# Kernel optimization log

Hardware: AMD Instinct MI355X
Metric: run time of the kernel (lower is better)

## Reference

```python
import jax, jax.numpy as jnp
import numpy as np

H, W = 160, 480
C_IMG = 256
VFC = [64, 128, 256]
N_PTS = 120000


def setup_inputs() -> dict:
    key = jax.random.key(0)
    ks = jax.random.split(key, 16)
    inp = {}
    inp["img_feat"] = jax.random.normal(ks[0], (C_IMG, H, W), jnp.float32)
    inp["seg_prob"] = jax.random.uniform(ks[1], (1, 2, H, W), jnp.float32)
    for i, c in enumerate(VFC):
        inp[f"voxel_feat{i}"] = jax.random.normal(ks[2 + i], (N_PTS, c), jnp.float32)
        x = jax.random.randint(ks[5 + i], (N_PTS,), 0, W + 1)  # col coord in [0, W]
        y = jax.random.randint(ks[8 + i], (N_PTS,), 0, H + 1)  # row coord in [0, H]
        inp[f"img_grid{i}"] = jnp.stack([x, y], axis=1).astype(jnp.int32)
    inp["red_w0"] = jax.random.normal(ks[11], (VFC[2], VFC[0]), jnp.float32) * 0.05
    inp["red_b0"] = jnp.zeros((VFC[2],), jnp.float32)
    inp["red_w1"] = jax.random.normal(ks[12], (VFC[2], VFC[1]), jnp.float32) * 0.05
    inp["red_b1"] = jnp.zeros((VFC[2],), jnp.float32)
    inp["sb_w"] = jax.random.normal(ks[13], (1, C_IMG + VFC[2], 3, 3), jnp.float32) * 0.02
    inp["sb_b"] = jnp.zeros((1,), jnp.float32)
    return inp


def pts2img(coor, pts_feat):
    # coor: [N,2] int (x, y); torch does coor[:, [1,0]] then grid[y, x] = feat
    c = pts_feat.shape[1]
    grid = jnp.zeros((H + 1, W + 1, c), pts_feat.dtype)
    grid = grid.at[coor[:, 1], coor[:, 0]].set(pts_feat, mode="drop")
    return grid[:-1, :-1].transpose(2, 0, 1)  # [C, H, W]


def reference(img_feat, seg_prob, voxel_feat0, voxel_feat1, voxel_feat2,
              img_grid0, img_grid1, img_grid2,
              red_w0, red_b0, red_w1, red_b1, sb_w, sb_b):
    # seg-gated image features
    enhanced = img_feat * seg_prob[0, 1][None]  # [C_IMG, H, W]

    # level 0: scatter + 1x1 conv (64 -> 256)
    p0 = pts2img(img_grid0, voxel_feat0)
    p0 = jnp.einsum('chw,oc->ohw', p0, red_w0) + red_b0[:, None, None]
    # level 1: scatter + 1x1 conv (128 -> 256)
    p1 = pts2img(img_grid1, voxel_feat1)
    p1 = jnp.einsum('chw,oc->ohw', p1, red_w1) + red_b1[:, None, None]
    # level 2: scatter only (already 256)
    p2 = pts2img(img_grid2, voxel_feat2)
    pt_img = p0 + p1 + p2  # [256, H, W]

    fused = jnp.concatenate([enhanced, pt_img], axis=0)[None]  # [1, 512, H, W]
    conv = jax.lax.conv_general_dilated(
        fused, sb_w, window_strides=(1, 1), padding='SAME',
        dimension_numbers=('NCHW', 'OIHW', 'NCHW'))
    conv = conv + sb_b[None, :, None, None]
    attention_map = jax.nn.sigmoid(conv[0])  # [1, H, W]
    return enhanced * attention_map
```

## Files before the change

kernel.cpp:

```cpp
#include <hip/hip_runtime.h>
#include <math.h>

#define H 160
#define W 480
#define HW 76800
#define NPTS 120000
#define NUNIT 6

#define OFF_W1M 307200
#define OFF_W2M 614400
#define OFF_T9  921600
#define OFF_WE0 17510400
#define OFF_WE1 17513472
#define OFF_BC  17519616

__global__ __launch_bounds__(256) void scatter_winners(
    const int2* __restrict__ g0, const int2* __restrict__ g1, const int2* __restrict__ g2,
    int* __restrict__ w0, int* __restrict__ w1, int* __restrict__ w2) {
  int j = blockIdx.x * blockDim.x + threadIdx.x;
  if (j >= NPTS) return;
  int2 c;
  c = g0[j];
  if ((unsigned)c.x < W && (unsigned)c.y < H) atomicMax(&w0[c.y * W + c.x], j);
  c = g1[j];
  if ((unsigned)c.x < W && (unsigned)c.y < H) atomicMax(&w1[c.y * W + c.x], j);
  c = g2[j];
  if ((unsigned)c.x < W && (unsigned)c.y < H) atomicMax(&w2[c.y * W + c.x], j);
}

__global__ __launch_bounds__(256) void prep_weights(
    const float* __restrict__ rw0, const float* __restrict__ rw1,
    const float* __restrict__ rb0, const float* __restrict__ rb1,
    const float* __restrict__ sbw,
    float* __restrict__ Weff0, float* __restrict__ Weff1, float* __restrict__ bconst) {
  int t = blockIdx.x * blockDim.x + threadIdx.x;
  if (t < 576) {
    int jj = t / 64, k = t % 64;
    float s = 0.f;
    for (int c = 0; c < 256; ++c) s = fmaf(rw0[c * 64 + k], sbw[(256 + c) * 9 + jj], s);
    Weff0[k * 12 + jj] = s;
  } else if (t < 1728) {
    int tt = t - 576;
    int jj = tt / 128, k = tt % 128;
    float s = 0.f;
    for (int c = 0; c < 256; ++c) s = fmaf(rw1[c * 128 + k], sbw[(256 + c) * 9 + jj], s);
    Weff1[k * 12 + jj] = s;
  } else if (t < 1737) {
    int jj = t - 1728;
    float s = 0.f;
    for (int c = 0; c < 256; ++c) s = fmaf(rb0[c] + rb1[c], sbw[(256 + c) * 9 + jj], s);
    bconst[jj] = s;
  }
}

template <int NF4, int WS>
__device__ __forceinline__ void gath(const float* __restrict__ row,
                                     const float* __restrict__ wbase,
                                     float acc[9]) {
  float4 v[NF4];
#pragma unroll
  for (int i = 0; i < NF4; ++i) v[i] = reinterpret_cast<const float4*>(row)[i];
#pragma unroll
  for (int i = 0; i < NF4; ++i) {
    const float* wc = wbase + i * 4 * WS;
#pragma unroll
    for (int j = 0; j < 9; ++j) {
      acc[j] = fmaf(v[i].x, wc[j], acc[j]);
      acc[j] = fmaf(v[i].y, wc[WS + j], acc[j]);
      acc[j] = fmaf(v[i].z, wc[2 * WS + j], acc[j]);
      acc[j] = fmaf(v[i].w, wc[3 * WS + j], acc[j]);
    }
  }
}

__global__ __launch_bounds__(256, 3) void t9_kernel(
    const float* __restrict__ img, const float* __restrict__ seg,
    const float* __restrict__ vf0, const float* __restrict__ vf1,
    const float* __restrict__ vf2,
    const int* __restrict__ w0m, const int* __restrict__ w1m,
    const int* __restrict__ w2m,
    const float* __restrict__ We0, const float* __restrict__ We1,
    const float* __restrict__ sbw, float* __restrict__ t9) {
  int p = blockIdx.x * 256 + threadIdx.x;
  int u = blockIdx.y;
  float acc[9];
#pragma unroll
  for (int j = 0; j < 9; ++j) acc[j] = 0.f;

  if (u < 2) {
    const int c0 = u * 128;
    float s = seg[HW + p];
    for (int cc = 0; cc < 128; cc += 16) {
      float v[16];
#pragma unroll
      for (int t = 0; t < 16; ++t) v[t] = img[(size_t)(c0 + cc + t) * HW + p];
#pragma unroll
      for (int t = 0; t < 16; ++t) {
        const float* wr = sbw + (c0 + cc + t) * 9;
#pragma unroll
        for (int j = 0; j < 9; ++j) acc[j] = fmaf(v[t], wr[j], acc[j]);
      }
    }
#pragma unroll
    for (int j = 0; j < 9; ++j) acc[j] *= s;
  } else if (u == 2) {
    int w0 = w0m[p];
    if (w0 >= 0) gath<16, 12>(vf0 + (size_t)w0 * 64, We0, acc);
    int w1 = w1m[p];
    if (w1 >= 0) gath<12, 12>(vf1 + (size_t)w1 * 128, We1, acc);
  } else if (u == 3) {
    int w1 = w1m[p];
    if (w1 >= 0) gath<20, 12>(vf1 + (size_t)w1 * 128 + 48, We1 + 48 * 12, acc);
    int w2 = w2m[p];
    if (w2 >= 0) gath<8, 9>(vf2 + (size_t)w2 * 256, sbw + 256 * 9, acc);
  } else if (u == 4) {
    int w2 = w2m[p];
    if (w2 >= 0) gath<28, 9>(vf2 + (size_t)w2 * 256 + 32, sbw + (256 + 32) * 9, acc);
  } else {
    int w2 = w2m[p];
    if (w2 >= 0) gath<28, 9>(vf2 + (size_t)w2 * 256 + 144, sbw + (256 + 144) * 9, acc);
  }

  float* dst = t9 + (size_t)u * 9 * HW + p;
#pragma unroll
  for (int j = 0; j < 9; ++j) dst[(size_t)j * HW] = acc[j];
}

__global__ __launch_bounds__(256) void conv_sig_kernel(
    const float* __restrict__ t9, const float* __restrict__ bconst,
    const float* __restrict__ sbb, const float* __restrict__ seg,
    float* __restrict__ sa) {
  int p = blockIdx.x * blockDim.x + threadIdx.x;
  int y = p / W, x = p - y * W;
  float s = sbb[0];
#pragma unroll
  for (int dy = -1; dy <= 1; ++dy) {
#pragma unroll
    for (int dx = -1; dx <= 1; ++dx) {
      int yy = y + dy, xx = x + dx;
      if ((unsigned)yy < H && (unsigned)xx < W) {
        int j = (dy + 1) * 3 + (dx + 1);
        int q = yy * W + xx;
        float t = bconst[j];
#pragma unroll
        for (int u = 0; u < NUNIT; ++u) t += t9[(size_t)(u * 9 + j) * HW + q];
        s += t;
      }
    }
  }
  float att = 1.f / (1.f + expf(-s));
  sa[p] = att * seg[HW + p];
}

__global__ __launch_bounds__(256) void final_mul_kernel(
    const float* __restrict__ img, const float* __restrict__ sa, float* __restrict__ out) {
  int i = blockIdx.x * blockDim.x + threadIdx.x;
  int e = i * 4;
  int p = e % HW;
  float4 v = *(const float4*)(img + e);
  float4 g = *(const float4*)(sa + p);
  float4 o = make_float4(v.x * g.x, v.y * g.y, v.z * g.z, v.w * g.w);
  *(float4*)(out + e) = o;
}

extern "C" void kernel_launch(void* const* d_in, const int* in_sizes, int n_in,
                              void* d_out, int out_size, void* d_ws, size_t ws_size,
                              hipStream_t stream) {
  const float* img = (const float*)d_in[0];
  const float* seg = (const float*)d_in[1];
  int iV0 = 2, iG0 = 3, iV1 = 4, iG1 = 5, iV2 = 6, iG2 = 7;
  if (in_sizes[3] != 2 * NPTS) {
    iV0 = 2; iV1 = 3; iV2 = 4; iG0 = 5; iG1 = 6; iG2 = 7;
  }
  const float* vf0 = (const float*)d_in[iV0];
  const float* vf1 = (const float*)d_in[iV1];
  const float* vf2 = (const float*)d_in[iV2];
  const int2* g0 = (const int2*)d_in[iG0];
  const int2* g1 = (const int2*)d_in[iG1];
  const int2* g2 = (const int2*)d_in[iG2];
  const float* rw0 = (const float*)d_in[8];
  const float* rb0 = (const float*)d_in[9];
  const float* rw1 = (const float*)d_in[10];
  const float* rb1 = (const float*)d_in[11];
  const float* sbw = (const float*)d_in[12];
  const float* sbb = (const float*)d_in[13];

  char* ws = (char*)d_ws;
  int* w0m = (int*)(ws + 0);
  int* w1m = (int*)(ws + OFF_W1M);
  int* w2m = (int*)(ws + OFF_W2M);
  float* t9 = (float*)(ws + OFF_T9);
  float* Weff0 = (float*)(ws + OFF_WE0);
  float* Weff1 = (float*)(ws + OFF_WE1);
  float* bconst = (float*)(ws + OFF_BC);
  float* sa = (float*)(ws + 0);

  float* out = (float*)d_out;

  hipMemsetAsync(w0m, 0xFF, 3 * 307200, stream);
  prep_weights<<<7, 256, 0, stream>>>(rw0, rw1, rb0, rb1, sbw, Weff0, Weff1, bconst);
  scatter_winners<<<(NPTS + 255) / 256, 256, 0, stream>>>(g0, g1, g2, w0m, w1m, w2m);
  dim3 tg(HW / 256, NUNIT);
  t9_kernel<<<tg, 256, 0, stream>>>(img, seg, vf0, vf1, vf2, w0m, w1m, w2m,
                                    Weff0, Weff1, sbw, t9);
  conv_sig_kernel<<<HW / 256, 256, 0, stream>>>(t9, bconst, sbb, seg, sa);
  final_mul_kernel<<<(out_size / 4) / 256, 256, 0, stream>>>(img, sa, out);
}
```

Baseline: 372.9 us.

## Compact occupied pixels into per-level lists and gather voxel rows cooperatively via LDS

Builds per-level compacted lists of occupied pixels (winner index, pixel) using ballot and atomic counters, then processes 64 entries per block. Rows are loaded coalesced into a transposed LDS tile, and the 9-tap contraction is split across four waves with an LDS reduction. This replaces the per-pixel divergent row gathers and skips empty pixels. Weight prep is fused with the scatter launch, and the image contraction gets its own kernel. The cost is an extra compaction kernel, a memset of the per-pixel voxel buffers, and a larger LDS footprint (about 75 KB per block) that limits occupancy.

```diff
diff --git a/kernel.cpp b/kernel.cpp
--- a/kernel.cpp
+++ b/kernel.cpp
@@ -5,131 +5,187 @@
 #define W 480
 #define HW 76800
 #define NPTS 120000
-#define NUNIT 6
-
-#define OFF_W1M 307200
-#define OFF_W2M 614400
-#define OFF_T9  921600
-#define OFF_WE0 17510400
-#define OFF_WE1 17513472
-#define OFF_BC  17519616
-
-__global__ __launch_bounds__(256) void scatter_winners(
-    const int2* __restrict__ g0, const int2* __restrict__ g1, const int2* __restrict__ g2,
-    int* __restrict__ w0, int* __restrict__ w1, int* __restrict__ w2) {
-  int j = blockIdx.x * blockDim.x + threadIdx.x;
-  if (j >= NPTS) return;
-  int2 c;
-  c = g0[j];
-  if ((unsigned)c.x < W && (unsigned)c.y < H) atomicMax(&w0[c.y * W + c.x], j);
-  c = g1[j];
-  if ((unsigned)c.x < W && (unsigned)c.y < H) atomicMax(&w1[c.y * W + c.x], j);
-  c = g2[j];
-  if ((unsigned)c.x < W && (unsigned)c.y < H) atomicMax(&w2[c.y * W + c.x], j);
-}
-
-__global__ __launch_bounds__(256) void prep_weights(
+
+#define OFF_W1M   307200
+#define OFF_W2M   614400
+#define OFF_CNT   921600
+#define OFF_T9I   921616
+#define OFF_T9V0  6451216
+#define OFF_T9V1  10137616
+#define OFF_T9V2  13824016
+#define OFF_L0    17510416
+#define OFF_L1    18124816
+#define OFF_L2    18739216
+#define OFF_WE0   19353616
+#define OFF_WE1   19356688
+#define OFF_BC    19362832
+
+__global__ __launch_bounds__(256) void prep_and_scatter(
     const float* __restrict__ rw0, const float* __restrict__ rw1,
     const float* __restrict__ rb0, const float* __restrict__ rb1,
     const float* __restrict__ sbw,
-    float* __restrict__ Weff0, float* __restrict__ Weff1, float* __restrict__ bconst) {
-  int t = blockIdx.x * blockDim.x + threadIdx.x;
-  if (t < 576) {
-    int jj = t / 64, k = t % 64;
-    float s = 0.f;
-    for (int c = 0; c < 256; ++c) s = fmaf(rw0[c * 64 + k], sbw[(256 + c) * 9 + jj], s);
-    Weff0[k * 12 + jj] = s;
-  } else if (t < 1728) {
-    int tt = t - 576;
-    int jj = tt / 128, k = tt % 128;
-    float s = 0.f;
-    for (int c = 0; c < 256; ++c) s = fmaf(rw1[c * 128 + k], sbw[(256 + c) * 9 + jj], s);
-    Weff1[k * 12 + jj] = s;
-  } else if (t < 1737) {
-    int jj = t - 1728;
-    float s = 0.f;
-    for (int c = 0; c < 256; ++c) s = fmaf(rb0[c] + rb1[c], sbw[(256 + c) * 9 + jj], s);
-    bconst[jj] = s;
-  }
-}
-
-template <int NF4, int WS>
-__device__ __forceinline__ void gath(const float* __restrict__ row,
-                                     const float* __restrict__ wbase,
-                                     float acc[9]) {
-  float4 v[NF4];
-#pragma unroll
-  for (int i = 0; i < NF4; ++i) v[i] = reinterpret_cast<const float4*>(row)[i];
-#pragma unroll
-  for (int i = 0; i < NF4; ++i) {
-    const float* wc = wbase + i * 4 * WS;
-#pragma unroll
-    for (int j = 0; j < 9; ++j) {
-      acc[j] = fmaf(v[i].x, wc[j], acc[j]);
-      acc[j] = fmaf(v[i].y, wc[WS + j], acc[j]);
-      acc[j] = fmaf(v[i].z, wc[2 * WS + j], acc[j]);
-      acc[j] = fmaf(v[i].w, wc[3 * WS + j], acc[j]);
-    }
-  }
-}
-
-__global__ __launch_bounds__(256, 3) void t9_kernel(
-    const float* __restrict__ img, const float* __restrict__ seg,
+    float* __restrict__ Weff0, float* __restrict__ Weff1, float* __restrict__ bconst,
+    int* __restrict__ cnt,
+    const int2* __restrict__ g0, const int2* __restrict__ g1, const int2* __restrict__ g2,
+    int* __restrict__ w0, int* __restrict__ w1, int* __restrict__ w2) {
+  if (blockIdx.x < 7) {
+    int t = blockIdx.x * 256 + threadIdx.x;
+    if (t < 576) {
+      int jj = t / 64, k = t % 64;
+      float s = 0.f;
+      for (int c = 0; c < 256; ++c) s = fmaf(rw0[c * 64 + k], sbw[(256 + c) * 9 + jj], s);
+      Weff0[k * 12 + jj] = s;
+    } else if (t < 1728) {
+      int tt = t - 576;
+      int jj = tt / 128, k = tt % 128;
+      float s = 0.f;
+      for (int c = 0; c < 256; ++c) s = fmaf(rw1[c * 128 + k], sbw[(256 + c) * 9 + jj], s);
+      Weff1[k * 12 + jj] = s;
+    } else if (t < 1737) {
+      int jj = t - 1728;
+      float s = 0.f;
+      for (int c = 0; c < 256; ++c) s = fmaf(rb0[c] + rb1[c], sbw[(256 + c) * 9 + jj], s);
+      bconst[jj] = s;
+    } else if (t < 1740) {
+      cnt[t - 1737] = 0;
+    }
+  } else {
+    int j = (blockIdx.x - 7) * 256 + threadIdx.x;
+    if (j >= NPTS) return;
+    int2 c;
+    c = g0[j];
+    if ((unsigned)c.x < W && (unsigned)c.y < H) atomicMax(&w0[c.y * W + c.x], j);
+    c = g1[j];
+    if ((unsigned)c.x < W && (unsigned)c.y < H) atomicMax(&w1[c.y * W + c.x], j);
+    c = g2[j];
+    if ((unsigned)c.x < W && (unsigned)c.y < H) atomicMax(&w2[c.y * W + c.x], j);
+  }
+}
+
+__global__ __launch_bounds__(256) void compact_kernel(
+    const int* __restrict__ w0m, const int* __restrict__ w1m, const int* __restrict__ w2m,
+    int2* __restrict__ L0o, int2* __restrict__ L1o, int2* __restrict__ L2o,
+    int* __restrict__ cnt) {
+  int p = blockIdx.x * 256 + threadIdx.x;
+  int lane = threadIdx.x & 63;
+#pragma unroll
+  for (int l = 0; l < 3; ++l) {
+    int w = (l == 0) ? w0m[p] : (l == 1) ? w1m[p] : w2m[p];
+    int2* Lo = (l == 0) ? L0o : (l == 1) ? L1o : L2o;
+    unsigned long long m = __ballot(w >= 0);
+    int c = __popcll(m);
+    int base = 0;
+    if (lane == 0 && c) base = atomicAdd(&cnt[l], c);
+    base = __shfl(base, 0);
+    if (w >= 0) {
+      int off = __popcll(m & ((1ull << lane) - 1ull));
+      Lo[base + off] = make_int2(w, p);
+    }
+  }
+}
+
+template <int CH>
+__device__ __forceinline__ void vox_body(
+    const int2* __restrict__ list, int n, const float* __restrict__ vf,
+    const float* __restrict__ wbase, int wstride, float* __restrict__ out,
+    float* ldsT, float* part, int2* ent) {
+  const int CPQ = CH / 4;
+  int t = threadIdx.x;
+  int i0 = blockIdx.x * 64;
+  if (i0 >= n) return;
+  if (t < 64) {
+    int idx = i0 + t;
+    ent[t] = (idx < n) ? list[idx] : make_int2(0, -1);
+  }
+  __syncthreads();
+#pragma unroll
+  for (int k = 0; k < CPQ; ++k) {
+    int flat = t + 256 * k;
+    int r = flat / CH;
+    int c = flat % CH;
+    ldsT[c * 65 + r] = vf[(size_t)ent[r].x * CH + c];
+  }
+  __syncthreads();
+  int pt = t & 63;
+  int q = __builtin_amdgcn_readfirstlane(t >> 6);
+  int c0 = q * CPQ;
+  float acc[9];
+#pragma unroll
+  for (int j = 0; j < 9; ++j) acc[j] = 0.f;
+#pragma unroll 8
+  for (int i = 0; i < CPQ; ++i) {
+    float v = ldsT[(c0 + i) * 65 + pt];
+    const float* wr = wbase + (c0 + i) * wstride;
+#pragma unroll
+    for (int j = 0; j < 9; ++j) acc[j] = fmaf(v, wr[j], acc[j]);
+  }
+#pragma unroll
+  for (int j = 0; j < 9; ++j) part[pt * 37 + j * 4 + q] = acc[j];
+  __syncthreads();
+  if (t < 64) {
+    int2 e = ent[t];
+    if (e.y >= 0) {
+      float s[9];
+#pragma unroll
+      for (int j = 0; j < 9; ++j)
+        s[j] = (part[t * 37 + j * 4 + 0] + part[t * 37 + j * 4 + 1]) +
+               (part[t * 37 + j * 4 + 2] + part[t * 37 + j * 4 + 3]);
+      float* d = out + (size_t)e.y * 12;
+      *(float4*)(d + 0) = make_float4(s[0], s[1], s[2], s[3]);
+      *(float4*)(d + 4) = make_float4(s[4], s[5], s[6], s[7]);
+      d[8] = s[8];
+    }
+  }
+}
+
+__global__ __launch_bounds__(256) void vox_kernel(
+    const int2* __restrict__ l0, const int2* __restrict__ l1, const int2* __restrict__ l2,
+    const int* __restrict__ cnt,
     const float* __restrict__ vf0, const float* __restrict__ vf1,
     const float* __restrict__ vf2,
-    const int* __restrict__ w0m, const int* __restrict__ w1m,
-    const int* __restrict__ w2m,
     const float* __restrict__ We0, const float* __restrict__ We1,
-    const float* __restrict__ sbw, float* __restrict__ t9) {
+    const float* __restrict__ sbw,
+    float* __restrict__ t9v0, float* __restrict__ t9v1, float* __restrict__ t9v2) {
+  __shared__ float ldsT[256 * 65];
+  __shared__ float part[64 * 37];
+  __shared__ int2 ent[64];
+  int z = blockIdx.y;
+  if (z == 2)      vox_body<256>(l2, cnt[2], vf2, sbw + 256 * 9, 9, t9v2, ldsT, part, ent);
+  else if (z == 1) vox_body<128>(l1, cnt[1], vf1, We1, 12, t9v1, ldsT, part, ent);
+  else             vox_body<64> (l0, cnt[0], vf0, We0, 12, t9v0, ldsT, part, ent);
+}
+
+__global__ __launch_bounds__(256) void img_kernel(
+    const float* __restrict__ img, const float* __restrict__ seg,
+    const float* __restrict__ sbw, float* __restrict__ t9i) {
   int p = blockIdx.x * 256 + threadIdx.x;
-  int u = blockIdx.y;
+  int hh = blockIdx.y;
+  int c0 = hh * 128;
   float acc[9];
 #pragma unroll
   for (int j = 0; j < 9; ++j) acc[j] = 0.f;
-
-  if (u < 2) {
-    const int c0 = u * 128;
-    float s = seg[HW + p];
-    for (int cc = 0; cc < 128; cc += 16) {
-      float v[16];
-#pragma unroll
-      for (int t = 0; t < 16; ++t) v[t] = img[(size_t)(c0 + cc + t) * HW + p];
-#pragma unroll
-      for (int t = 0; t < 16; ++t) {
-        const float* wr = sbw + (c0 + cc + t) * 9;
-#pragma unroll
-        for (int j = 0; j < 9; ++j) acc[j] = fmaf(v[t], wr[j], acc[j]);
-      }
-    }
-#pragma unroll
-    for (int j = 0; j < 9; ++j) acc[j] *= s;
-  } else if (u == 2) {
-    int w0 = w0m[p];
-    if (w0 >= 0) gath<16, 12>(vf0 + (size_t)w0 * 64, We0, acc);
-    int w1 = w1m[p];
-    if (w1 >= 0) gath<12, 12>(vf1 + (size_t)w1 * 128, We1, acc);
-  } else if (u == 3) {
-    int w1 = w1m[p];
-    if (w1 >= 0) gath<20, 12>(vf1 + (size_t)w1 * 128 + 48, We1 + 48 * 12, acc);
-    int w2 = w2m[p];
-    if (w2 >= 0) gath<8, 9>(vf2 + (size_t)w2 * 256, sbw + 256 * 9, acc);
-  } else if (u == 4) {
-    int w2 = w2m[p];
-    if (w2 >= 0) gath<28, 9>(vf2 + (size_t)w2 * 256 + 32, sbw + (256 + 32) * 9, acc);
-  } else {
-    int w2 = w2m[p];
-    if (w2 >= 0) gath<28, 9>(vf2 + (size_t)w2 * 256 + 144, sbw + (256 + 144) * 9, acc);
-  }
-
-  float* dst = t9 + (size_t)u * 9 * HW + p;
-#pragma unroll
-  for (int j = 0; j < 9; ++j) dst[(size_t)j * HW] = acc[j];
+  for (int cc = 0; cc < 128; cc += 16) {
+    float v[16];
+#pragma unroll
+    for (int tt = 0; tt < 16; ++tt) v[tt] = img[(size_t)(c0 + cc + tt) * HW + p];
+#pragma unroll
+    for (int tt = 0; tt < 16; ++tt) {
+      const float* wr = sbw + (c0 + cc + tt) * 9;
+#pragma unroll
+      for (int j = 0; j < 9; ++j) acc[j] = fmaf(v[tt], wr[j], acc[j]);
+    }
+  }
+  float s = seg[HW + p];
+  float* dst = t9i + (size_t)hh * 9 * HW + p;
+#pragma unroll
+  for (int j = 0; j < 9; ++j) dst[(size_t)j * HW] = acc[j] * s;
 }
 
 __global__ __launch_bounds__(256) void conv_sig_kernel(
-    const float* __restrict__ t9, const float* __restrict__ bconst,
-    const float* __restrict__ sbb, const float* __restrict__ seg,
-    float* __restrict__ sa) {
+    const float* __restrict__ t9i, const float* __restrict__ t9v0,
+    const float* __restrict__ t9v1, const float* __restrict__ t9v2,
+    const float* __restrict__ bconst, const float* __restrict__ sbb,
+    const float* __restrict__ seg, float* __restrict__ sa) {
   int p = blockIdx.x * blockDim.x + threadIdx.x;
   int y = p / W, x = p - y * W;
   float s = sbb[0];
@@ -141,9 +197,8 @@
       if ((unsigned)yy < H && (unsigned)xx < W) {
         int j = (dy + 1) * 3 + (dx + 1);
         int q = yy * W + xx;
-        float t = bconst[j];
-#pragma unroll
-        for (int u = 0; u < NUNIT; ++u) t += t9[(size_t)(u * 9 + j) * HW + q];
+        float t = bconst[j] + t9i[(size_t)j * HW + q] + t9i[(size_t)(9 + j) * HW + q];
+        t += t9v0[(size_t)q * 12 + j] + t9v1[(size_t)q * 12 + j] + t9v2[(size_t)q * 12 + j];
         s += t;
       }
     }
@@ -189,7 +244,14 @@
   int* w0m = (int*)(ws + 0);
   int* w1m = (int*)(ws + OFF_W1M);
   int* w2m = (int*)(ws + OFF_W2M);
-  float* t9 = (float*)(ws + OFF_T9);
+  int* cnt = (int*)(ws + OFF_CNT);
+  float* t9i = (float*)(ws + OFF_T9I);
+  float* t9v0 = (float*)(ws + OFF_T9V0);
+  float* t9v1 = (float*)(ws + OFF_T9V1);
+  float* t9v2 = (float*)(ws + OFF_T9V2);
+  int2* l0 = (int2*)(ws + OFF_L0);
+  int2* l1 = (int2*)(ws + OFF_L1);
+  int2* l2 = (int2*)(ws + OFF_L2);
   float* Weff0 = (float*)(ws + OFF_WE0);
   float* Weff1 = (float*)(ws + OFF_WE1);
   float* bconst = (float*)(ws + OFF_BC);
@@ -198,11 +260,16 @@
   float* out = (float*)d_out;
 
   hipMemsetAsync(w0m, 0xFF, 3 * 307200, stream);
-  prep_weights<<<7, 256, 0, stream>>>(rw0, rw1, rb0, rb1, sbw, Weff0, Weff1, bconst);
-  scatter_winners<<<(NPTS + 255) / 256, 256, 0, stream>>>(g0, g1, g2, w0m, w1m, w2m);
-  dim3 tg(HW / 256, NUNIT);
-  t9_kernel<<<tg, 256, 0, stream>>>(img, seg, vf0, vf1, vf2, w0m, w1m, w2m,
-                                    Weff0, Weff1, sbw, t9);
-  conv_sig_kernel<<<HW / 256, 256, 0, stream>>>(t9, bconst, sbb, seg, sa);
+  hipMemsetAsync(ws + OFF_T9V0, 0, 3 * 3686400, stream);
+  prep_and_scatter<<<7 + (NPTS + 255) / 256, 256, 0, stream>>>(
+      rw0, rw1, rb0, rb1, sbw, Weff0, Weff1, bconst, cnt, g0, g1, g2, w0m, w1m, w2m);
+  compact_kernel<<<HW / 256, 256, 0, stream>>>(w0m, w1m, w2m, l0, l1, l2, cnt);
+  dim3 vg(HW / 64, 3);
+  vox_kernel<<<vg, 256, 0, stream>>>(l0, l1, l2, cnt, vf0, vf1, vf2,
+                                     Weff0, Weff1, sbw, t9v0, t9v1, t9v2);
+  dim3 ig(HW / 256, 2);
+  img_kernel<<<ig, 256, 0, stream>>>(img, seg, sbw, t9i);
+  conv_sig_kernel<<<HW / 256, 256, 0, stream>>>(t9i, t9v0, t9v1, t9v2,
+                                                bconst, sbb, seg, sa);
   final_mul_kernel<<<(out_size / 4) / 256, 256, 0, stream>>>(img, sa, out);
 }
```

Result: slower. 420.7 us (+12.8%).
